# Kernel optimization log

Hardware: AMD Instinct MI355X
Metric: run time of the kernel (lower is better)

The kernel has to match this reference:

```python
import jax, jax.numpy as jnp
import numpy as np

B, I, D, H, DP = 2, 256, 768, 12, 128
DK = D // H  # 64
NPQ, NPV = 4, 8  # query/key points and value points per head


def setup_inputs() -> dict:
    key = jax.random.key(0)
    ks = jax.random.split(key, 24)
    s = 0.02
    w = lambda k, shp: (jax.random.normal(k, shp, jnp.float32) * s)
    inp = {
        "x1d": jax.random.normal(ks[0], (B, I, D), jnp.float32),
        "x2d": jax.random.normal(ks[1], (B, I, I, DP), jnp.float32),
        "past_T": jax.random.normal(ks[2], (B, I, 3), jnp.float32),
        "past_R": jax.random.normal(ks[3], (B, I, 3, 3), jnp.float32),
        "last_T": jax.random.normal(ks[4], (B, I, 3), jnp.float32),
        "last_R": jax.random.normal(ks[5], (B, I, 3, 3), jnp.float32),
        "bias": jax.random.normal(ks[6], (B, H, I, I), jnp.float32) * 0.1,
        "Wq": w(ks[7], (D, D)),
        "Wk": w(ks[8], (D, D)),
        "Wv": w(ks[9], (D, D)),
        "W_pair_bias": w(ks[10], (DP, H)),
        "Wpq_past": w(ks[11], (D, H * NPQ * 3)),
        "Wpk_past": w(ks[12], (D, H * NPQ * 3)),
        "Wpv_past": w(ks[13], (D, H * NPV * 3)),
        "Wpq_last": w(ks[14], (D, H * NPQ * 3)),
        "Wpk_last": w(ks[15], (D, H * NPQ * 3)),
        "Wpv_last": w(ks[16], (D, H * NPV * 3)),
        "tpw_past": jax.random.uniform(ks[17], (H,), jnp.float32),
        "tpw_last": jax.random.uniform(ks[18], (H,), jnp.float32),
        "W_pair_value": w(ks[19], (DP, D)),
        "W_out": w(ks[20], (2 * D + 2 * H * 8 * 4, D)),
        "b_out": jnp.zeros((D,), jnp.float32),
    }
    return inp


def reference(x1d, x2d, past_T, past_R, last_T, last_R, bias,
              Wq, Wk, Wv, W_pair_bias,
              Wpq_past, Wpk_past, Wpv_past,
              Wpq_last, Wpk_last, Wpv_last,
              tpw_past, tpw_last, W_pair_value, W_out, b_out):
    b, i, d = x1d.shape
    h = tpw_past.shape[0]
    dk = d // h
    scalar_w = 1.0 / np.sqrt(3.0 * dk)
    point_w = 1.0 / np.sqrt(3.0 * 4.0 * 9.0 / 2.0)
    pair_w = 1.0 / np.sqrt(3.0)

    # scalar attention
    q = (x1d @ Wq).reshape(b, i, h, dk)
    k = (x1d @ Wk).reshape(b, i, h, dk)
    v = (x1d @ Wv).reshape(b, i, h, dk)
    scalar_attn = jnp.einsum('bihc,bjhc->bhij', q * scalar_w, k)

    past_IR = jnp.swapaxes(past_R, -1, -2)
    last_IR = jnp.swapaxes(last_R, -1, -2)

    def affine(pts, T, IR):  # pts: [b,i,h,c,3]
        return jnp.einsum('bipq,bihcq->bihcp', IR, pts) + T[:, :, None, None, :]

    def point_branch(Wpq, Wpk, Wpv, T, IR, tpw):
        qp = (x1d @ Wpq).reshape(b, i, h, NPQ, 3)
        kp = (x1d @ Wpk).reshape(b, i, h, NPQ, 3)
        vp = (x1d @ Wpv).reshape(b, i, h, NPV, 3)
        qg, kg, vg = affine(qp, T, IR), affine(kp, T, IR), affine(vp, T, IR)
        # pairwise point distances: [b,i,j,h,NPQ]
        dist = jnp.linalg.norm(qg[:, :, None] - kg[:, None], axis=-1)
        pw = point_w * jax.nn.softplus(tpw)  # [h]
        attn = -0.5 * pw[:, None, None] * jnp.transpose(dist.sum(-1), (0, 3, 1, 2))
        return attn, vg

    pa_past, vg_past = point_branch(Wpq_past, Wpk_past, Wpv_past, past_T, past_IR, tpw_past)
    pa_last, vg_last = point_branch(Wpq_last, Wpk_last, Wpv_last, last_T, last_IR, tpw_last)

    pair_attn = pair_w * jnp.transpose(x2d @ W_pair_bias, (0, 3, 1, 2))  # bhij

    attn = jax.nn.softmax(scalar_attn + pa_past + pa_last + pair_attn + bias, axis=-1)

    out_scalar = jnp.einsum('bhij,bjhc->bihc', attn, v).reshape(b, i, d)
    og_past = jnp.einsum('bhij,bjhcp->bihcp', attn, vg_past)
    og_last = jnp.einsum('bhij,bjhcp->bihcp', attn, vg_last)

    # NOTE: the original module inverts BOTH branches with the PAST pose (faithful).
    def inv_past(og):
        return jnp.einsum('bipq,bihcq->bihcp', past_R, og - past_T[:, :, None, None, :])

    ol_past = inv_past(og_past)
    ol_last = inv_past(og_last)
    n_past = jnp.linalg.norm(ol_past, axis=-1).reshape(b, i, h * NPV)
    n_last = jnp.linalg.norm(ol_last, axis=-1).reshape(b, i, h * NPV)
    ol_past = ol_past.reshape(b, i, h * NPV * 3)
    ol_last = ol_last.reshape(b, i, h * NPV * 3)

    v_pair = (x2d @ W_pair_value).reshape(b, i, i, h, dk)
    out_pair = jnp.einsum('bhij,bijhc->bihc', attn, v_pair).reshape(b, i, d)

    feat = jnp.concatenate([out_pair, out_scalar, ol_past, n_past, ol_last, n_last], axis=-1)
    return feat @ W_out + b_out  # dropout is identity at eval
```

## Files before the change

kernel.cpp:

```cpp
#include <hip/hip_runtime.h>
#include <hip/hip_bf16.h>
#include <math.h>

#define BB 2
#define II 256
#define DD 768
#define HH 12
#define DPP 128
#define NPQ 4
#define NPV 8
#define FEAT_DIM 2304
#define NPACK 3456

#define OFF_QKVPTS ((size_t)0)
#define OFF_PBATTN ((size_t)1769472)
#define OFF_X1DB   ((size_t)3342336)
#define OFF_VT     OFF_X1DB
#define OFF_W1T    ((size_t)3538944)
#define OFF_ABF    OFF_W1T
#define OFF_W2T    ((size_t)4866048)
#define OFF_FEATB  ((size_t)5750784)
#define OFF_QPTS   ((size_t)6340608)
#define OFF_KPTS   ((size_t)6488064)
#define OFF_X2DT   ((size_t)6635520)
#define OFF_QKHM   ((size_t)15024128)
#define OFF_VGJT   ((size_t)15417344)
#define OFF_WPVT   ((size_t)15564800)

#define SCALAR_W 0.07216878364870323f
#define POINT_W  0.13608276348795434f
#define PAIR_W   0.57735026918962576f

typedef __attribute__((ext_vector_type(8))) short short8;
typedef __attribute__((ext_vector_type(4))) short short4v;
typedef __attribute__((ext_vector_type(4))) float f32x4;
typedef __attribute__((ext_vector_type(16))) float f32x16;

__device__ inline ushort f2bf(float f) {
  __hip_bfloat16 h = __float2bfloat16(f);
  return *reinterpret_cast<ushort*>(&h);
}
__device__ inline float bf2f(short u) {
  return __uint_as_float(((unsigned int)(unsigned short)u) << 16);
}

__global__ __launch_bounds__(256)
void convert_x_kernel(const float* __restrict__ src, ushort* __restrict__ dst, int n8) {
  const int idx = blockIdx.x * 256 + threadIdx.x;
  if (idx >= n8) return;
  const float4 f0 = reinterpret_cast<const float4*>(src)[idx * 2 + 0];
  const float4 f1 = reinterpret_cast<const float4*>(src)[idx * 2 + 1];
  short8 v;
  v[0] = (short)f2bf(f0.x); v[1] = (short)f2bf(f0.y);
  v[2] = (short)f2bf(f0.z); v[3] = (short)f2bf(f0.w);
  v[4] = (short)f2bf(f1.x); v[5] = (short)f2bf(f1.y);
  v[6] = (short)f2bf(f1.z); v[7] = (short)f2bf(f1.w);
  reinterpret_cast<short8*>(dst)[idx] = v;
}

struct TJob { const float* src; ushort* dst; int K, N, sStride, dStride; };
struct TJobs { TJob j[11]; };

__global__ __launch_bounds__(256)
void transpose_pack_kernel(TJobs jobs) {
  const TJob J = jobs.j[blockIdx.z];
  const int k0 = blockIdx.y * 32, n0 = blockIdx.x * 32;
  if (k0 >= J.K || n0 >= J.N) return;
  __shared__ float t[32][33];
  const int tid = threadIdx.x;
  const int c = tid & 31, r = tid >> 5;
#pragma unroll
  for (int u = 0; u < 4; ++u) {
    const int kk = r + u * 8;
    t[kk][c] = (n0 + c < J.N) ? J.src[(size_t)(k0 + kk) * J.sStride + n0 + c] : 0.f;
  }
  __syncthreads();
#pragma unroll
  for (int u = 0; u < 4; ++u) {
    const int n = n0 + r + u * 8;
    if (n < J.N) J.dst[(size_t)n * J.dStride + k0 + c] = f2bf(t[c][r + u * 8]);
  }
}

__global__ __launch_bounds__(256)
void mfma_gemm_kernel(const ushort* __restrict__ A, const ushort* __restrict__ Bt,
                      float* __restrict__ C, const float* __restrict__ bias,
                      ushort* __restrict__ Cb, ushort* __restrict__ Vt, int N, int K) {
  __shared__ short a_s[64 * 64];
  __shared__ short b_s[64 * 64];
  const int tid = threadIdx.x;
  const int lane = tid & 63;
  const int wave = tid >> 6;
  const int wm = wave >> 1, wn = wave & 1;
  const int m0 = blockIdx.x * 64, n0 = blockIdx.y * 64;
  const int lrow = tid >> 3, lch = tid & 7;
  const int l15 = lane & 15, l7 = lane & 7, kq = lane >> 4;
  f32x4 acc[2][2] = {};
  for (int kc = 0; kc < K; kc += 64) {
#pragma unroll
    for (int u = 0; u < 2; ++u) {
      const int r = lrow + u * 32;
      const short8 av = *reinterpret_cast<const short8*>(A  + (size_t)(m0 + r) * K + kc + lch * 8);
      const short8 bv = *reinterpret_cast<const short8*>(Bt + (size_t)(n0 + r) * K + kc + lch * 8);
      const int sc = ((lch ^ (r & 7)) << 3);
      *reinterpret_cast<short8*>(&a_s[r * 64 + sc]) = av;
      *reinterpret_cast<short8*>(&b_s[r * 64 + sc]) = bv;
    }
    __syncthreads();
#pragma unroll
    for (int kk = 0; kk < 64; kk += 32) {
      const int ch = (kk >> 3) + kq;
      const int cx = ((ch ^ l7) << 3);
      short8 af[2], bf[2];
      af[0] = *reinterpret_cast<const short8*>(&a_s[(wm * 32 +      l15) * 64 + cx]);
      af[1] = *reinterpret_cast<const short8*>(&a_s[(wm * 32 + 16 + l15) * 64 + cx]);
      bf[0] = *reinterpret_cast<const short8*>(&b_s[(wn * 32 +      l15) * 64 + cx]);
      bf[1] = *reinterpret_cast<const short8*>(&b_s[(wn * 32 + 16 + l15) * 64 + cx]);
#pragma unroll
      for (int mt = 0; mt < 2; ++mt)
#pragma unroll
        for (int nt = 0; nt < 2; ++nt)
          acc[mt][nt] = __builtin_amdgcn_mfma_f32_16x16x32_bf16(af[mt], bf[nt], acc[mt][nt], 0, 0, 0);
    }
    __syncthreads();
  }
#pragma unroll
  for (int mt = 0; mt < 2; ++mt) {
    const int r0 = m0 + wm * 32 + mt * 16 + kq * 4;
#pragma unroll
    for (int nt = 0; nt < 2; ++nt) {
      const int c = n0 + wn * 32 + nt * 16 + l15;
      const float bv = bias ? bias[c] : 0.f;
#pragma unroll
      for (int rr = 0; rr < 4; ++rr) {
        const float val = acc[mt][nt][rr] + bv;
        const int m = r0 + rr;
        if (!Cb) {
          C[(size_t)m * N + c] = val;
        } else if (c < 1536) {
          const int bb = m >> 8, ii = m & 255;
          const int plane = (c >= 768) ? 1 : 0;
          const int hh = (c & 767) >> 6, cc2 = c & 63;
          Cb[((((size_t)plane * BB + bb) * HH + hh) * II + ii) * 64 + cc2] = f2bf(val);
        } else if (c < 2304) {
          const int bb = m >> 8, ii = m & 255;
          Vt[((size_t)bb * DD + (c - 1536)) * II + ii] = f2bf(val);
        } else {
          C[(size_t)m * N + c] = val;
        }
      }
    }
  }
}

struct XfJob { const float* T; const float* R; float* dstf; ushort* dstb;
               int np; int sub; int srccol; int mode; };
struct XfJobs { XfJob j[6]; };

__global__ __launch_bounds__(256)
void transform_kernel(const float* __restrict__ qkvpts, XfJobs jobs) {
  const XfJob J = jobs.j[blockIdx.y];
  const int idx = blockIdx.x * 256 + threadIdx.x;
  if (J.mode == 1) {
    const int hn = HH * J.np;
    if (idx >= BB * II * hn) return;
    const int bi = idx / hn, rem = idx - bi * hn;
    const float* p = qkvpts + (size_t)bi * NPACK + J.srccol + rem * 3;
    const float p0 = p[0], p1 = p[1], p2 = p[2];
    const float* R = J.R + (size_t)bi * 9;
    const float* T = J.T + (size_t)bi * 3;
    const float o0 = R[0] * p0 + R[3] * p1 + R[6] * p2 + T[0];
    const float o1 = R[1] * p0 + R[4] * p1 + R[7] * p2 + T[1];
    const float o2 = R[2] * p0 + R[5] * p1 + R[8] * p2 + T[2];
    const int h = rem / J.np, n = rem - h * J.np;
    const int b = bi >> 8, i = bi & 255;
    float* d = J.dstf + ((size_t)(b * HH + h) * II + i) * 24 + J.sub + n * 3;
    d[0] = o0; d[1] = o1; d[2] = o2;
  } else {
    if (idx >= BB * HH * J.np * II) return;
    const int i = idx & 255;
    int r2 = idx >> 8;
    const int n = r2 % J.np; r2 /= J.np;
    const int h = r2 % HH;
    const int b = r2 / HH;
    const int bi = b * II + i;
    const float* p = qkvpts + (size_t)bi * NPACK + J.srccol + (h * J.np + n) * 3;
    const float p0 = p[0], p1 = p[1], p2 = p[2];
    const float* R = J.R + (size_t)bi * 9;
    const float* T = J.T + (size_t)bi * 3;
    const float o0 = R[0] * p0 + R[3] * p1 + R[6] * p2 + T[0];
    const float o1 = R[1] * p0 + R[4] * p1 + R[7] * p2 + T[1];
    const float o2 = R[2] * p0 + R[5] * p1 + R[8] * p2 + T[2];
    if (J.mode == 2) {
      const int col = J.sub + h * 24 + n * 3;
      ushort* d = J.dstb + ((size_t)b * 576 + col) * II + i;
      d[0] = f2bf(o0); d[II] = f2bf(o1); d[2 * II] = f2bf(o2);
    } else {
      float* d = J.dstf + ((size_t)(b * HH + h) * 24 + J.sub + n * 3) * II + i;
      d[0] = o0; d[II] = o1; d[2 * II] = o2;
    }
  }
}

__global__ __launch_bounds__(256)
void x2d_pack_kernel(const float* __restrict__ x2d, const float* __restrict__ Wpb,
                     const float* __restrict__ bias,
                     ushort* __restrict__ x2dt, ushort* __restrict__ pbattn) {
  __shared__ ushort tb[64 * 136];
  __shared__ ushort wpbT_s[16 * 136];
  __shared__ ushort pb_red[128 * 18];
  const int tid = threadIdx.x;
  const int bi = blockIdx.x;
  const int half = blockIdx.y;
  const int b = bi >> 8, i = bi & 255;
  for (int u = tid; u < 2048; u += 256) {
    const int h = u >> 7, p = u & 127;
    wpbT_s[h * 136 + p] = (h < 12) ? f2bf(Wpb[p * 12 + h]) : (ushort)0;
  }
  const int lane = tid & 63, w = tid >> 6;
  const int l15 = lane & 15, kq = lane >> 4;
  for (int jtl = 0; jtl < 2; ++jtl) {
    const int jt = half * 2 + jtl;
    if (jtl) __syncthreads();
    const float4* src = reinterpret_cast<const float4*>(x2d + ((size_t)bi * II + jt * 64) * DPP);
#pragma unroll
    for (int u = 0; u < 8; ++u) {
      const int fid = tid + u * 256;
      const int j = fid >> 5, p4 = (fid & 31) * 4;
      const float4 v = src[fid];
      short4v o;
      o[0] = (short)f2bf(v.x); o[1] = (short)f2bf(v.y);
      o[2] = (short)f2bf(v.z); o[3] = (short)f2bf(v.w);
      *reinterpret_cast<short4v*>(&tb[j * 136 + (p4 ^ ((j >> 3) << 4))]) = o;
    }
    __syncthreads();
    {
      const int r = w * 16 + l15;
      const int rs = (r >> 3) << 4;
      f32x4 acc = {};
#pragma unroll
      for (int kk = 0; kk < 4; ++kk) {
        const short8 af = *reinterpret_cast<const short8*>(
            &tb[r * 136 + ((kk * 32 + kq * 8) ^ rs)]);
        const short8 bf = *reinterpret_cast<const short8*>(
            &wpbT_s[l15 * 136 + kk * 32 + kq * 8]);
        acc = __builtin_amdgcn_mfma_f32_16x16x32_bf16(af, bf, acc, 0, 0, 0);
      }
#pragma unroll
      for (int rr = 0; rr < 4; ++rr)
        pb_red[(jtl * 64 + w * 16 + kq * 4 + rr) * 18 + l15] = f2bf(acc[rr]);
    }
    {
      ushort* dst = x2dt + ((size_t)bi * 4 + jt) * (128 * 64);
#pragma unroll
      for (int u = 0; u < 4; ++u) {
        const int c = tid + u * 256;
        const int p = c >> 3, j0 = (c & 7) * 8;
        const int t = c & 7;
        const int pp = p ^ (t << 4);
        short8 o;
#pragma unroll
        for (int e = 0; e < 8; ++e) o[e] = (short)tb[(j0 + e) * 136 + pp];
        *reinterpret_cast<short8*>(&dst[(size_t)p * 64 + j0]) = o;
      }
    }
  }
  __syncthreads();
  {
    const int u = tid;
    if (u < 192) {
      const int h = u >> 4, jq = u & 15;
      const int j0 = half * 128 + jq * 8;
      const size_t base = (((size_t)(b * HH + h) * II + i) * II) + j0;
      const float4 bv0 = *reinterpret_cast<const float4*>(bias + base);
      const float4 bv1 = *reinterpret_cast<const float4*>(bias + base + 4);
      const float bv[8] = {bv0.x, bv0.y, bv0.z, bv0.w, bv1.x, bv1.y, bv1.z, bv1.w};
      short8 o;
#pragma unroll
      for (int e = 0; e < 8; ++e)
        o[e] = (short)f2bf(PAIR_W * bf2f((short)pb_red[(jq * 8 + e) * 18 + h]) + bv[e]);
      *reinterpret_cast<short8*>(pbattn + base) = o;
    }
  }
}

__global__ __launch_bounds__(256)
void attn_kernel(const ushort* __restrict__ qkhm,
                 const float* __restrict__ qpts, const float* __restrict__ kpts,
                 const float* __restrict__ tpw_past, const float* __restrict__ tpw_last,
                 const ushort* __restrict__ pbattn, ushort* __restrict__ abf) {
  __shared__ float qp_s[16 * 24];
  __shared__ float pb_s[16 * 260];
  __shared__ float red_s[2][16 * 4];
  __shared__ ushort a_lds[16 * 264];
  const int tid = threadIdx.x;
  const int lane = tid & 63;
  const int w = tid >> 6;
  const int i0 = blockIdx.x * 16;
  const int h = blockIdx.y;
  const int b = blockIdx.z;
  const size_t bh = (size_t)b * HH + h;
  if (tid < 96)
    reinterpret_cast<float4*>(qp_s)[tid] =
        reinterpret_cast<const float4*>(qpts + (bh * II + i0) * 24)[tid];
  {
    const ushort* src = pbattn + (bh * II + i0) * II;
    for (int u = tid; u < 512; u += 256) {
      const int r = u >> 5, c8 = u & 31;
      const short8 v = *reinterpret_cast<const short8*>(src + (size_t)r * II + c8 * 8);
      float* d = &pb_s[r * 260 + c8 * 8];
#pragma unroll
      for (int e = 0; e < 8; ++e) d[e] = bf2f(v[e]);
    }
  }
  __syncthreads();
  const int l15 = lane & 15, kq = lane >> 4;
  const ushort* qrow = qkhm + (((size_t)b * HH + h) * II + i0 + l15) * 64;
  const ushort* kplane = qkhm + (((size_t)(BB + b) * HH + h) * II) * 64;
  const short8 af0 = *reinterpret_cast<const short8*>(qrow + kq * 8);
  const short8 af1 = *reinterpret_cast<const short8*>(qrow + 32 + kq * 8);
  const float pwp = 0.5f * POINT_W * log1pf(expf(tpw_past[h]));
  const float pwl = 0.5f * POINT_W * log1pf(expf(tpw_last[h]));
  const float* kpt = kpts + bh * 6144;
  float lg[4][4];
#pragma unroll
  for (int jb = 0; jb < 4; ++jb) {
    const int j = w * 64 + jb * 16 + l15;
    const ushort* krow = kplane + (size_t)j * 64;
    f32x4 acc = {};
    acc = __builtin_amdgcn_mfma_f32_16x16x32_bf16(
        af0, *reinterpret_cast<const short8*>(krow + kq * 8), acc, 0, 0, 0);
    acc = __builtin_amdgcn_mfma_f32_16x16x32_bf16(
        af1, *reinterpret_cast<const short8*>(krow + 32 + kq * 8), acc, 0, 0, 0);
    float kg[24];
#pragma unroll
    for (int c = 0; c < 24; ++c) kg[c] = kpt[c * 256 + j];
#pragma unroll
    for (int rr = 0; rr < 4; ++rr) {
      const int il = kq * 4 + rr;
      const float* qg = &qp_s[il * 24];
      float dp = 0.f, dl = 0.f;
#pragma unroll
      for (int n = 0; n < 4; ++n) {
        float dx = qg[n * 3] - kg[n * 3], dy = qg[n * 3 + 1] - kg[n * 3 + 1],
              dz = qg[n * 3 + 2] - kg[n * 3 + 2];
        dp += sqrtf(dx * dx + dy * dy + dz * dz);
        dx = qg[12 + n * 3] - kg[12 + n * 3]; dy = qg[12 + n * 3 + 1] - kg[12 + n * 3 + 1];
        dz = qg[12 + n * 3 + 2] - kg[12 + n * 3 + 2];
        dl += sqrtf(dx * dx + dy * dy + dz * dz);
      }
      lg[jb][rr] = SCALAR_W * acc[rr] - pwp * dp - pwl * dl + pb_s[il * 260 + j];
    }
  }
#pragma unroll
  for (int rr = 0; rr < 4; ++rr) {
    float m = fmaxf(fmaxf(lg[0][rr], lg[1][rr]), fmaxf(lg[2][rr], lg[3][rr]));
    m = fmaxf(m, __shfl_xor(m, 1));
    m = fmaxf(m, __shfl_xor(m, 2));
    m = fmaxf(m, __shfl_xor(m, 4));
    m = fmaxf(m, __shfl_xor(m, 8));
    if (l15 == 0) red_s[0][(kq * 4 + rr) * 4 + w] = m;
  }
  __syncthreads();
#pragma unroll
  for (int rr = 0; rr < 4; ++rr) {
    const int il = kq * 4 + rr;
    const float* r = &red_s[0][il * 4];
    const float m = fmaxf(fmaxf(r[0], r[1]), fmaxf(r[2], r[3]));
    float s = 0.f;
#pragma unroll
    for (int jb = 0; jb < 4; ++jb) { lg[jb][rr] = __expf(lg[jb][rr] - m); s += lg[jb][rr]; }
    s += __shfl_xor(s, 1); s += __shfl_xor(s, 2);
    s += __shfl_xor(s, 4); s += __shfl_xor(s, 8);
    if (l15 == 0) red_s[1][il * 4 + w] = s;
  }
  __syncthreads();
#pragma unroll
  for (int rr = 0; rr < 4; ++rr) {
    const int il = kq * 4 + rr;
    const float* r = &red_s[1][il * 4];
    const float inv = 1.f / (r[0] + r[1] + r[2] + r[3]);
#pragma unroll
    for (int jb = 0; jb < 4; ++jb)
      a_lds[il * 264 + w * 64 + jb * 16 + l15] = f2bf(lg[jb][rr] * inv);
  }
  __syncthreads();
  ushort* ab = abf + (bh * II + i0) * II;
#pragma unroll
  for (int u = 0; u < 2; ++u) {
    const int idx = tid + u * 256;
    const int r = idx >> 5, cc = idx & 31;
    *reinterpret_cast<short8*>(ab + (size_t)r * II + cc * 8) =
        *reinterpret_cast<const short8*>(&a_lds[r * 264 + cc * 8]);
  }
}

__global__ __launch_bounds__(256)
void wpair_kernel(const ushort* __restrict__ x2dt, const ushort* __restrict__ abf,
                  const ushort* __restrict__ wpvt, ushort* __restrict__ featb) {
  __shared__ ushort a_s[16 * 256];
  __shared__ float t_s[16][128];
  const int tid = threadIdx.x;
  const int bi = blockIdx.x;
  const int b = bi >> 8, i = bi & 255;
#pragma unroll
  for (int u = 0; u < 2; ++u) {
    const int c = tid + u * 256;
    const int h = c >> 5, ch = c & 31;
    short8 v = {};
    if (h < 12)
      v = *reinterpret_cast<const short8*>(abf + (((size_t)(b * HH + h) * II + i) * II) + ch * 8);
    *reinterpret_cast<short8*>(&a_s[h * 256 + ((ch ^ h) << 3)]) = v;
  }
  __syncthreads();
  const int lane = tid & 63, w = tid >> 6;
  const int l15 = lane & 15, kq = lane >> 4;
  const int n0 = w * 32;
  const ushort* slab = x2dt + (size_t)bi * 32768;
  f32x4 acc[2] = {};
#pragma unroll
  for (int nt = 0; nt < 2; ++nt) {
    const int p = n0 + nt * 16 + l15;
#pragma unroll
    for (int ks = 0; ks < 8; ++ks) {
      const int j0 = ks * 32 + kq * 8;
      const short8 bf = *reinterpret_cast<const short8*>(
          &slab[((size_t)(j0 >> 6) * 128 + p) * 64 + (j0 & 63)]);
      const int ch32 = j0 >> 3;
      const short8 af = *reinterpret_cast<const short8*>(&a_s[l15 * 256 + ((ch32 ^ l15) << 3)]);
      acc[nt] = __builtin_amdgcn_mfma_f32_16x16x32_bf16(af, bf, acc[nt], 0, 0, 0);
    }
  }
#pragma unroll
  for (int nt = 0; nt < 2; ++nt) {
    const int p = n0 + nt * 16 + l15;
#pragma unroll
    for (int r = 0; r < 4; ++r) t_s[kq * 4 + r][p] = acc[nt][r];
  }
  __syncthreads();
  ushort* fout = featb + (size_t)bi * FEAT_DIM;
#pragma unroll
  for (int u = 0; u < 3; ++u) {
    const int c = tid + u * 256;
    const int h = c >> 6;
    const ushort* wr = wpvt + (size_t)c * DPP;
    float o = 0.f;
    for (int p = 0; p < DPP; p += 8) {
      const short8 wv = *reinterpret_cast<const short8*>(wr + p);
#pragma unroll
      for (int e = 0; e < 8; ++e) o += t_s[h][p + e] * bf2f(wv[e]);
    }
    fout[c] = f2bf(o);
  }
}

__global__ __launch_bounds__(256)
void av_kernel(const ushort* __restrict__ abf, const ushort* __restrict__ vt,
               const ushort* __restrict__ vgjt,
               const float* __restrict__ past_T, const float* __restrict__ past_R,
               ushort* __restrict__ featb) {
  __shared__ ushort a_s[32 * 256];
  __shared__ float c_s[32][116];
  const int tid = threadIdx.x;
  const int it = blockIdx.x;
  const int h  = blockIdx.y;
  const int b  = blockIdx.z;
  const int i0 = it * 32;
  const size_t bh = (size_t)b * HH + h;
  {
    const ushort* src = abf + (bh * II + i0) * II;
#pragma unroll
    for (int u = 0; u < 4; ++u) {
      const int cidx = tid + u * 256;
      const int r = cidx >> 5, ch = cidx & 31;
      const short8 v = *reinterpret_cast<const short8*>(src + (size_t)r * II + ch * 8);
      *reinterpret_cast<short8*>(&a_s[r * 256 + ((ch ^ (r & 7)) << 3)]) = v;
    }
  }
  __syncthreads();
  const int lane = tid & 63, w = tid >> 6;
  const int l15 = lane & 15, kq = lane >> 4;
  for (int t = w; t < 14; t += 4) {
    const int mt = t / 7, nt = t % 7;
    const int c = nt * 16 + l15;
    const ushort* bcol;
    if (c < 64)      bcol = vt   + ((size_t)b * DD + h * 64 + c) * II;
    else if (c < 88) bcol = vgjt + ((size_t)b * 576 + h * 24 + (c - 64)) * II;
    else             bcol = vgjt + ((size_t)b * 576 + 288 + h * 24 + (c - 88)) * II;
    f32x4 acc = {};
#pragma unroll
    for (int ks = 0; ks < 8; ++ks) {
      const int ch = ks * 4 + kq;
      const int r = mt * 16 + l15;
      const short8 af = *reinterpret_cast<const short8*>(&a_s[r * 256 + ((ch ^ (r & 7)) << 3)]);
      const short8 bf = *reinterpret_cast<const short8*>(bcol + ks * 32 + kq * 8);
      acc = __builtin_amdgcn_mfma_f32_16x16x32_bf16(af, bf, acc, 0, 0, 0);
    }
#pragma unroll
    for (int rr = 0; rr < 4; ++rr) c_s[mt * 16 + kq * 4 + rr][c] = acc[rr];
  }
  __syncthreads();
  {
    const int il = tid >> 3, c0 = (tid & 7) * 8;
    ushort* fo = featb + (size_t)(b * II + i0 + il) * FEAT_DIM + 768 + h * 64 + c0;
    short8 o;
#pragma unroll
    for (int e = 0; e < 8; ++e) o[e] = (short)f2bf(c_s[il][c0 + e]);
    *reinterpret_cast<short8*>(fo) = o;
  }
  for (int u = tid; u < 512; u += 256) {
    const int il = u >> 4;
    const int br = (u >> 3) & 1;
    const int n = u & 7;
    const int bi = b * II + i0 + il;
    const float* T = past_T + (size_t)bi * 3;
    const float* R = past_R + (size_t)bi * 9;
    const int cb = 64 + br * 24 + n * 3;
    const float o0 = c_s[il][cb + 0] - T[0];
    const float o1 = c_s[il][cb + 1] - T[1];
    const float o2 = c_s[il][cb + 2] - T[2];
    const float l0 = R[0] * o0 + R[1] * o1 + R[2] * o2;
    const float l1 = R[3] * o0 + R[4] * o1 + R[5] * o2;
    const float l2 = R[6] * o0 + R[7] * o1 + R[8] * o2;
    const float nn = sqrtf(l0 * l0 + l1 * l1 + l2 * l2);
    const int r = h * 8 + n;
    ushort* fout = featb + (size_t)bi * FEAT_DIM;
    const int olbase = br ? 1920 : 1536;
    const int nbase  = br ? 2208 : 1824;
    fout[olbase + r * 3 + 0] = f2bf(l0);
    fout[olbase + r * 3 + 1] = f2bf(l1);
    fout[olbase + r * 3 + 2] = f2bf(l2);
    fout[nbase + r] = f2bf(nn);
  }
}

extern "C" void kernel_launch(void* const* d_in, const int* in_sizes, int n_in,
                              void* d_out, int out_size, void* d_ws, size_t ws_size,
                              hipStream_t stream) {
  (void)in_sizes; (void)n_in; (void)out_size; (void)ws_size;
  const float* x1d      = (const float*)d_in[0];
  const float* x2d      = (const float*)d_in[1];
  const float* past_T   = (const float*)d_in[2];
  const float* past_R   = (const float*)d_in[3];
  const float* last_T   = (const float*)d_in[4];
  const float* last_R   = (const float*)d_in[5];
  const float* bias     = (const float*)d_in[6];
  const float* Wq       = (const float*)d_in[7];
  const float* Wk       = (const float*)d_in[8];
  const float* Wv       = (const float*)d_in[9];
  const float* Wpb      = (const float*)d_in[10];
  const float* Wpq_past = (const float*)d_in[11];
  const float* Wpk_past = (const float*)d_in[12];
  const float* Wpv_past = (const float*)d_in[13];
  const float* Wpq_last = (const float*)d_in[14];
  const float* Wpk_last = (const float*)d_in[15];
  const float* Wpv_last = (const float*)d_in[16];
  const float* tpw_past = (const float*)d_in[17];
  const float* tpw_last = (const float*)d_in[18];
  const float* W_pair_value = (const float*)d_in[19];
  const float* W_out    = (const float*)d_in[20];
  const float* b_out    = (const float*)d_in[21];
  float* out = (float*)d_out;
  float* ws  = (float*)d_ws;

  float*  qkvpts = ws + OFF_QKVPTS;
  ushort* pbattn = (ushort*)(ws + OFF_PBATTN);
  ushort* x1db   = (ushort*)(ws + OFF_X1DB);
  ushort* vt     = (ushort*)(ws + OFF_VT);
  ushort* w1t    = (ushort*)(ws + OFF_W1T);
  ushort* abf    = (ushort*)(ws + OFF_ABF);
  ushort* w2t    = (ushort*)(ws + OFF_W2T);
  ushort* featb  = (ushort*)(ws + OFF_FEATB);
  float*  qpts   = ws + OFF_QPTS;
  float*  kpts   = ws + OFF_KPTS;
  ushort* x2dt   = (ushort*)(ws + OFF_X2DT);
  ushort* qkhm   = (ushort*)(ws + OFF_QKHM);
  ushort* vgjt   = (ushort*)(ws + OFF_VGJT);
  ushort* wpvt   = (ushort*)(ws + OFF_WPVT);

  const dim3 blk256(256);

  x2d_pack_kernel<<<dim3(BB * II, 2), blk256, 0, stream>>>(x2d, Wpb, bias, x2dt, pbattn);

  convert_x_kernel<<<dim3(192), blk256, 0, stream>>>(x1d, x1db, 512 * 768 / 8);

  {
    TJobs jobs = {};
    jobs.j[0]  = {Wq,       w1t + (size_t)   0 * 768, DD,      DD,   DD,  768};
    jobs.j[1]  = {Wk,       w1t + (size_t) 768 * 768, DD,      DD,   DD,  768};
    jobs.j[2]  = {Wv,       w1t + (size_t)1536 * 768, DD,      DD,   DD,  768};
    jobs.j[3]  = {Wpq_past, w1t + (size_t)2304 * 768, DD,     144,   144, 768};
    jobs.j[4]  = {Wpk_past, w1t + (size_t)2448 * 768, DD,     144,   144, 768};
    jobs.j[5]  = {Wpv_past, w1t + (size_t)2592 * 768, DD,     288,   288, 768};
    jobs.j[6]  = {Wpq_last, w1t + (size_t)2880 * 768, DD,     144,   144, 768};
    jobs.j[7]  = {Wpk_last, w1t + (size_t)3024 * 768, DD,     144,   144, 768};
    jobs.j[8]  = {Wpv_last, w1t + (size_t)3168 * 768, DD,     288,   288, 768};
    jobs.j[9]  = {W_out,    w2t,                      FEAT_DIM, DD,  DD,  2304};
    jobs.j[10] = {W_pair_value, wpvt,                 DPP,     DD,   DD,  DPP};
    transpose_pack_kernel<<<dim3(24, 72, 11), blk256, 0, stream>>>(jobs);
  }

  mfma_gemm_kernel<<<dim3(8, 54), blk256, 0, stream>>>(
      x1db, w1t, qkvpts, nullptr, qkhm, vt, NPACK, DD);

  {
    XfJobs jobs = {};
    jobs.j[0] = {past_T, past_R, qpts, nullptr, NPQ,   0, 2304, 1};
    jobs.j[1] = {past_T, past_R, kpts, nullptr, NPQ,   0, 2448, 3};
    jobs.j[2] = {past_T, past_R, nullptr, vgjt, NPV,   0, 2592, 2};
    jobs.j[3] = {last_T, last_R, qpts, nullptr, NPQ,  12, 2880, 1};
    jobs.j[4] = {last_T, last_R, kpts, nullptr, NPQ,  12, 3024, 3};
    jobs.j[5] = {last_T, last_R, nullptr, vgjt, NPV, 288, 3168, 2};
    transform_kernel<<<dim3(192, 6), blk256, 0, stream>>>(qkvpts, jobs);
  }

  attn_kernel<<<dim3(16, HH, BB), blk256, 0, stream>>>(
      qkhm, qpts, kpts, tpw_past, tpw_last, pbattn, abf);

  wpair_kernel<<<dim3(BB * II), blk256, 0, stream>>>(x2dt, abf, wpvt, featb);

  av_kernel<<<dim3(8, HH, BB), blk256, 0, stream>>>(
      abf, vt, vgjt, past_T, past_R, featb);

  mfma_gemm_kernel<<<dim3(8, 12), blk256, 0, stream>>>(
      featb, w2t, out, b_out, nullptr, nullptr, DD, FEAT_DIM);
}
```

Before: 122.2 us.

## Drop bf16 x2d transposed workspace; read fp32 x2d directly in pair kernels

Removes the intermediate transposed bf16 copy of x2d (about 16 MB written, then read back). The pair-bias kernel now loads fp32 x2d rows straight into MFMA operands, and the pair-value kernel re-reads fp32 x2d and converts and transposes it through LDS itself. This trades the workspace write and read for a second pass over the 64 MB fp32 x2d. It also adds strided scalar LDS gathers for the B operand in wpair.

```diff
diff --git a/kernel.cpp b/kernel.cpp
--- a/kernel.cpp
+++ b/kernel.cpp
@@ -22,10 +22,9 @@
 #define OFF_FEATB  ((size_t)5750784)
 #define OFF_QPTS   ((size_t)6340608)
 #define OFF_KPTS   ((size_t)6488064)
-#define OFF_X2DT   ((size_t)6635520)
-#define OFF_QKHM   ((size_t)15024128)
-#define OFF_VGJT   ((size_t)15417344)
-#define OFF_WPVT   ((size_t)15564800)
+#define OFF_QKHM   ((size_t)6635520)
+#define OFF_VGJT   ((size_t)7028736)
+#define OFF_WPVT   ((size_t)7176192)
 
 #define SCALAR_W 0.07216878364870323f
 #define POINT_W  0.13608276348795434f
@@ -203,12 +202,10 @@
 }
 
 __global__ __launch_bounds__(256)
-void x2d_pack_kernel(const float* __restrict__ x2d, const float* __restrict__ Wpb,
-                     const float* __restrict__ bias,
-                     ushort* __restrict__ x2dt, ushort* __restrict__ pbattn) {
-  __shared__ ushort tb[64 * 136];
+void pairbias_kernel(const float* __restrict__ x2d, const float* __restrict__ Wpb,
+                     const float* __restrict__ bias, ushort* __restrict__ pbattn) {
   __shared__ ushort wpbT_s[16 * 136];
-  __shared__ ushort pb_red[128 * 18];
+  __shared__ ushort pb_s[128 * 18];
   const int tid = threadIdx.x;
   const int bi = blockIdx.x;
   const int half = blockIdx.y;
@@ -217,70 +214,45 @@
     const int h = u >> 7, p = u & 127;
     wpbT_s[h * 136 + p] = (h < 12) ? f2bf(Wpb[p * 12 + h]) : (ushort)0;
   }
+  __syncthreads();
   const int lane = tid & 63, w = tid >> 6;
   const int l15 = lane & 15, kq = lane >> 4;
-  for (int jtl = 0; jtl < 2; ++jtl) {
-    const int jt = half * 2 + jtl;
-    if (jtl) __syncthreads();
-    const float4* src = reinterpret_cast<const float4*>(x2d + ((size_t)bi * II + jt * 64) * DPP);
-#pragma unroll
-    for (int u = 0; u < 8; ++u) {
-      const int fid = tid + u * 256;
-      const int j = fid >> 5, p4 = (fid & 31) * 4;
-      const float4 v = src[fid];
-      short4v o;
-      o[0] = (short)f2bf(v.x); o[1] = (short)f2bf(v.y);
-      o[2] = (short)f2bf(v.z); o[3] = (short)f2bf(v.w);
-      *reinterpret_cast<short4v*>(&tb[j * 136 + (p4 ^ ((j >> 3) << 4))]) = o;
-    }
-    __syncthreads();
-    {
-      const int r = w * 16 + l15;
-      const int rs = (r >> 3) << 4;
-      f32x4 acc = {};
-#pragma unroll
-      for (int kk = 0; kk < 4; ++kk) {
-        const short8 af = *reinterpret_cast<const short8*>(
-            &tb[r * 136 + ((kk * 32 + kq * 8) ^ rs)]);
-        const short8 bf = *reinterpret_cast<const short8*>(
-            &wpbT_s[l15 * 136 + kk * 32 + kq * 8]);
-        acc = __builtin_amdgcn_mfma_f32_16x16x32_bf16(af, bf, acc, 0, 0, 0);
-      }
-#pragma unroll
-      for (int rr = 0; rr < 4; ++rr)
-        pb_red[(jtl * 64 + w * 16 + kq * 4 + rr) * 18 + l15] = f2bf(acc[rr]);
-    }
-    {
-      ushort* dst = x2dt + ((size_t)bi * 4 + jt) * (128 * 64);
-#pragma unroll
-      for (int u = 0; u < 4; ++u) {
-        const int c = tid + u * 256;
-        const int p = c >> 3, j0 = (c & 7) * 8;
-        const int t = c & 7;
-        const int pp = p ^ (t << 4);
-        short8 o;
-#pragma unroll
-        for (int e = 0; e < 8; ++e) o[e] = (short)tb[(j0 + e) * 136 + pp];
-        *reinterpret_cast<short8*>(&dst[(size_t)p * 64 + j0]) = o;
-      }
-    }
-  }
-  __syncthreads();
-  {
-    const int u = tid;
-    if (u < 192) {
-      const int h = u >> 4, jq = u & 15;
-      const int j0 = half * 128 + jq * 8;
-      const size_t base = (((size_t)(b * HH + h) * II + i) * II) + j0;
-      const float4 bv0 = *reinterpret_cast<const float4*>(bias + base);
-      const float4 bv1 = *reinterpret_cast<const float4*>(bias + base + 4);
-      const float bv[8] = {bv0.x, bv0.y, bv0.z, bv0.w, bv1.x, bv1.y, bv1.z, bv1.w};
-      short8 o;
-#pragma unroll
-      for (int e = 0; e < 8; ++e)
-        o[e] = (short)f2bf(PAIR_W * bf2f((short)pb_red[(jq * 8 + e) * 18 + h]) + bv[e]);
-      *reinterpret_cast<short8*>(pbattn + base) = o;
-    }
+  const float* xbase = x2d + ((size_t)bi * II + half * 128) * DPP;
+#pragma unroll
+  for (int mi = 0; mi < 2; ++mi) {
+    const int mt = w + mi * 4;
+    const int jl = mt * 16 + l15;
+    const float* arow = xbase + (size_t)jl * DPP;
+    f32x4 acc = {};
+#pragma unroll
+    for (int kk = 0; kk < 4; ++kk) {
+      const float4 f0 = *reinterpret_cast<const float4*>(arow + kk * 32 + kq * 8);
+      const float4 f1 = *reinterpret_cast<const float4*>(arow + kk * 32 + kq * 8 + 4);
+      short8 af;
+      af[0] = (short)f2bf(f0.x); af[1] = (short)f2bf(f0.y);
+      af[2] = (short)f2bf(f0.z); af[3] = (short)f2bf(f0.w);
+      af[4] = (short)f2bf(f1.x); af[5] = (short)f2bf(f1.y);
+      af[6] = (short)f2bf(f1.z); af[7] = (short)f2bf(f1.w);
+      const short8 bf = *reinterpret_cast<const short8*>(&wpbT_s[l15 * 136 + kk * 32 + kq * 8]);
+      acc = __builtin_amdgcn_mfma_f32_16x16x32_bf16(af, bf, acc, 0, 0, 0);
+    }
+#pragma unroll
+    for (int rr = 0; rr < 4; ++rr)
+      pb_s[(mt * 16 + kq * 4 + rr) * 18 + l15] = f2bf(acc[rr]);
+  }
+  __syncthreads();
+  if (tid < 192) {
+    const int h = tid >> 4, jq = tid & 15;
+    const int jl0 = jq * 8;
+    const size_t base = (((size_t)(b * HH + h) * II + i) * II) + half * 128 + jl0;
+    const float4 bv0 = *reinterpret_cast<const float4*>(bias + base);
+    const float4 bv1 = *reinterpret_cast<const float4*>(bias + base + 4);
+    const float bv[8] = {bv0.x, bv0.y, bv0.z, bv0.w, bv1.x, bv1.y, bv1.z, bv1.w};
+    short8 o;
+#pragma unroll
+    for (int e = 0; e < 8; ++e)
+      o[e] = (short)f2bf(PAIR_W * bf2f((short)pb_s[(jl0 + e) * 18 + h]) + bv[e]);
+    *reinterpret_cast<short8*>(pbattn + base) = o;
   }
 }
 
@@ -396,9 +368,10 @@
 }
 
 __global__ __launch_bounds__(256)
-void wpair_kernel(const ushort* __restrict__ x2dt, const ushort* __restrict__ abf,
+void wpair_kernel(const float* __restrict__ x2d, const ushort* __restrict__ abf,
                   const ushort* __restrict__ wpvt, ushort* __restrict__ featb) {
   __shared__ ushort a_s[16 * 256];
+  __shared__ ushort tb[64 * 136];
   __shared__ float t_s[16][128];
   const int tid = threadIdx.x;
   const int bi = blockIdx.x;
@@ -412,23 +385,39 @@
       v = *reinterpret_cast<const short8*>(abf + (((size_t)(b * HH + h) * II + i) * II) + ch * 8);
     *reinterpret_cast<short8*>(&a_s[h * 256 + ((ch ^ h) << 3)]) = v;
   }
-  __syncthreads();
   const int lane = tid & 63, w = tid >> 6;
   const int l15 = lane & 15, kq = lane >> 4;
   const int n0 = w * 32;
-  const ushort* slab = x2dt + (size_t)bi * 32768;
   f32x4 acc[2] = {};
-#pragma unroll
-  for (int nt = 0; nt < 2; ++nt) {
-    const int p = n0 + nt * 16 + l15;
-#pragma unroll
-    for (int ks = 0; ks < 8; ++ks) {
-      const int j0 = ks * 32 + kq * 8;
-      const short8 bf = *reinterpret_cast<const short8*>(
-          &slab[((size_t)(j0 >> 6) * 128 + p) * 64 + (j0 & 63)]);
-      const int ch32 = j0 >> 3;
-      const short8 af = *reinterpret_cast<const short8*>(&a_s[l15 * 256 + ((ch32 ^ l15) << 3)]);
-      acc[nt] = __builtin_amdgcn_mfma_f32_16x16x32_bf16(af, bf, acc[nt], 0, 0, 0);
+  for (int jt = 0; jt < 4; ++jt) {
+    __syncthreads();
+    const float4* src = reinterpret_cast<const float4*>(x2d + ((size_t)bi * II + jt * 64) * DPP);
+#pragma unroll
+    for (int u = 0; u < 8; ++u) {
+      const int fid = tid + u * 256;
+      const int j = fid >> 5, p4 = (fid & 31) * 4;
+      const float4 v = src[fid];
+      short4v o;
+      o[0] = (short)f2bf(v.x); o[1] = (short)f2bf(v.y);
+      o[2] = (short)f2bf(v.z); o[3] = (short)f2bf(v.w);
+      *reinterpret_cast<short4v*>(&tb[j * 136 + (p4 ^ ((j >> 3) << 4))]) = o;
+    }
+    __syncthreads();
+#pragma unroll
+    for (int nt = 0; nt < 2; ++nt) {
+      const int p = n0 + nt * 16 + l15;
+#pragma unroll
+      for (int kk = 0; kk < 2; ++kk) {
+        const int ch32 = jt * 8 + kk * 4 + kq;
+        const short8 af = *reinterpret_cast<const short8*>(&a_s[l15 * 256 + ((ch32 ^ l15) << 3)]);
+        short8 bf;
+#pragma unroll
+        for (int e = 0; e < 8; ++e) {
+          const int row = kk * 32 + kq * 8 + e;
+          bf[e] = (short)tb[row * 136 + (p ^ ((row >> 3) << 4))];
+        }
+        acc[nt] = __builtin_amdgcn_mfma_f32_16x16x32_bf16(af, bf, acc[nt], 0, 0, 0);
+      }
     }
   }
 #pragma unroll
@@ -573,14 +562,13 @@
   ushort* featb  = (ushort*)(ws + OFF_FEATB);
   float*  qpts   = ws + OFF_QPTS;
   float*  kpts   = ws + OFF_KPTS;
-  ushort* x2dt   = (ushort*)(ws + OFF_X2DT);
   ushort* qkhm   = (ushort*)(ws + OFF_QKHM);
   ushort* vgjt   = (ushort*)(ws + OFF_VGJT);
   ushort* wpvt   = (ushort*)(ws + OFF_WPVT);
 
   const dim3 blk256(256);
 
-  x2d_pack_kernel<<<dim3(BB * II, 2), blk256, 0, stream>>>(x2d, Wpb, bias, x2dt, pbattn);
+  pairbias_kernel<<<dim3(BB * II, 2), blk256, 0, stream>>>(x2d, Wpb, bias, pbattn);
 
   convert_x_kernel<<<dim3(192), blk256, 0, stream>>>(x1d, x1db, 512 * 768 / 8);
 
@@ -617,7 +605,7 @@
   attn_kernel<<<dim3(16, HH, BB), blk256, 0, stream>>>(
       qkhm, qpts, kpts, tpw_past, tpw_last, pbattn, abf);
 
-  wpair_kernel<<<dim3(BB * II), blk256, 0, stream>>>(x2dt, abf, wpvt, featb);
+  wpair_kernel<<<dim3(BB * II), blk256, 0, stream>>>(x2d, abf, wpvt, featb);
 
   av_kernel<<<dim3(8, HH, BB), blk256, 0, stream>>>(
       abf, vt, vgjt, past_T, past_R, featb);
```

After: 125.3 us. 1.03x slower.
